# Performance work log

Measured on AMD Instinct MI355X. Metric: run time of the kernel, lower is better.

The kernel has to match this reference:

```python
import jax, jax.numpy as jnp
import numpy as np
from jax import lax

DIM = 192
HEADS = 8
HIDDEN = int(DIM * 2.66)  # 510
EPS_LN = 1e-5
EPS_NORM = 1e-12


def conv1x1(x, w):
    # x: (B,C,H,W), w: (O,I,1,1)
    return lax.conv_general_dilated(x, w, (1, 1), 'VALID',
                                    dimension_numbers=('NCHW', 'OIHW', 'NCHW'))


def dwconv3x3(x, w):
    # depthwise 3x3, padding=1; w: (C,1,3,3)
    c = x.shape[1]
    return lax.conv_general_dilated(x, w, (1, 1), 'SAME',
                                    dimension_numbers=('NCHW', 'OIHW', 'NCHW'),
                                    feature_group_count=c)


def layernorm_chan(x, weight, bias):
    # WithBias LayerNorm over channel dim of NCHW (matches to_3d -> LN(-1) -> to_4d)
    mu = jnp.mean(x, axis=1, keepdims=True)
    var = jnp.var(x, axis=1, keepdims=True)
    xn = (x - mu) * lax.rsqrt(var + EPS_LN)
    return xn * weight[None, :, None, None] + bias[None, :, None, None]


def l2norm(x):
    # F.normalize along last dim with eps=1e-12
    n = jnp.sqrt(jnp.sum(x * x, axis=-1, keepdims=True))
    return x / jnp.maximum(n, EPS_NORM)


def attention(x, temperature, w_qkv, w_qkv_dw, w_proj):
    b, c, h, w = x.shape
    hw = h * w
    head_dim = c // HEADS
    qkv = dwconv3x3(conv1x1(x, w_qkv), w_qkv_dw)  # (B, 3C, H, W)
    q, k, v = jnp.split(qkv, 3, axis=1)
    q = l2norm(q.reshape(b, HEADS, head_dim, hw))
    k = l2norm(k.reshape(b, HEADS, head_dim, hw))
    v = v.reshape(b, HEADS, head_dim, hw)
    # channel-wise attention: (B,H,d,d)
    attn = jnp.einsum('bhde,bhce->bhdc', q, k) * temperature[None]
    attn = jax.nn.softmax(attn, axis=-1)
    out = jnp.einsum('bhdc,bhce->bhde', attn, v).reshape(b, c, h, w)
    return conv1x1(out, w_proj)


def ffn(x, w_in, w_dw, w_out):
    x = conv1x1(x, w_in)                 # (B, 2*hidden, H, W)
    x = dwconv3x3(x, w_dw)
    x1, x2 = jnp.split(x, 2, axis=1)
    x = jax.nn.gelu(x1, approximate=False) * x2
    return conv1x1(x, w_out)


def setup_inputs() -> dict:
    key = jax.random.key(0)
    ks = jax.random.split(key, 8)
    b, c, h, w = 4, DIM, 128, 128
    s = 0.05
    return {
        'x': jax.random.normal(ks[0], (b, c, h, w), jnp.float32),
        'temperature': jnp.ones((HEADS, 1, 1), jnp.float32),
        'ln1_w': jnp.ones((c,), jnp.float32),
        'ln1_b': jnp.zeros((c,), jnp.float32),
        'ln2_w': jnp.ones((c,), jnp.float32),
        'ln2_b': jnp.zeros((c,), jnp.float32),
        'w_qkv': jax.random.normal(ks[1], (3 * c, c, 1, 1), jnp.float32) * s,
        'w_qkv_dw': jax.random.normal(ks[2], (3 * c, 1, 3, 3), jnp.float32) * s,
        'w_proj': jax.random.normal(ks[3], (c, c, 1, 1), jnp.float32) * s,
        'w_in': jax.random.normal(ks[4], (2 * HIDDEN, c, 1, 1), jnp.float32) * s,
        'w_dw': jax.random.normal(ks[5], (2 * HIDDEN, 1, 3, 3), jnp.float32) * s,
        'w_out_ffn': jax.random.normal(ks[6], (c, HIDDEN, 1, 1), jnp.float32) * s,
    }


def reference(x, temperature, ln1_w, ln1_b, ln2_w, ln2_b, w_qkv, w_qkv_dw,
              w_proj, w_in, w_dw, w_out_ffn):
    x = x + attention(layernorm_chan(x, ln1_w, ln1_b), temperature,
                      w_qkv, w_qkv_dw, w_proj)
    x = x + ffn(layernorm_chan(x, ln2_w, ln2_b), w_in, w_dw, w_out_ffn)
    return x
```

## Files before the change

kernel.cpp:

```cpp
#include <hip/hip_runtime.h>
#include <hip/hip_bf16.h>
#include <math.h>


#define HW_ 16384

typedef __attribute__((ext_vector_type(8))) short bf16x8;
typedef __attribute__((ext_vector_type(4))) float f32x4;
typedef __attribute__((ext_vector_type(16))) float f32x16;
typedef __attribute__((ext_vector_type(4))) int i32x4;

union Pack8 { __hip_bfloat16 h[8]; i32x4 v; };

__global__ __launch_bounds__(256) void convert_weights(
    const float* __restrict__ wqkv, const float* __restrict__ wproj,
    const float* __restrict__ win, const float* __restrict__ wout,
    __hip_bfloat16* __restrict__ oq, __hip_bfloat16* __restrict__ op,
    __hip_bfloat16* __restrict__ oi, __hip_bfloat16* __restrict__ oo) {
  const int i = blockIdx.x * 256 + threadIdx.x;
  if (i < 110592) oq[i] = __float2bfloat16(wqkv[i]);
  if (i < 36864)  op[i] = __float2bfloat16(wproj[i]);
  if (i < 196608) {
    int m = i / 192, k = i - m * 192;
    oi[i] = __float2bfloat16(m < 1020 ? win[m * 192 + k] : 0.f);
  }
  if (i < 98304) {
    int m = i >> 9, k = i & 511;
    oo[i] = __float2bfloat16(k < 510 ? wout[m * 510 + k] : 0.f);
  }
}

__global__ __launch_bounds__(256) void ln_t_kernel(
    const float* __restrict__ x, const float* __restrict__ w,
    const float* __restrict__ bi, __hip_bfloat16* __restrict__ yt) {
  const int b = blockIdx.y;
  x += (size_t)b * 192 * HW_;
  yt += (size_t)b * HW_ * 192;
  __shared__ float tile[192][68];
  __shared__ float psum[4][64], psq[4][64];
  __shared__ float mu_s[64], inv_s[64];
  const int tid = threadIdx.x;
  const int p0 = blockIdx.x * 64;
  for (int idx = tid; idx < 192 * 16; idx += 256) {
    int c = idx >> 4, p4 = idx & 15;
    f32x4 v = *(const f32x4*)(x + (size_t)c * HW_ + p0 + p4 * 4);
    *(f32x4*)&tile[c][p4 * 4] = v;
  }
  __syncthreads();
  const int tx = tid & 63, ty = tid >> 6;
  float s = 0.f, s2 = 0.f;
  for (int c = ty * 48; c < ty * 48 + 48; c++) {
    float v = tile[c][tx]; s += v; s2 += v * v;
  }
  psum[ty][tx] = s; psq[ty][tx] = s2;
  __syncthreads();
  if (ty == 0) {
    float ts = psum[0][tx] + psum[1][tx] + psum[2][tx] + psum[3][tx];
    float ts2 = psq[0][tx] + psq[1][tx] + psq[2][tx] + psq[3][tx];
    float mu = ts * (1.f / 192.f);
    float var = ts2 * (1.f / 192.f) - mu * mu;
    mu_s[tx] = mu; inv_s[tx] = rsqrtf(var + 1e-5f);
  }
  __syncthreads();
  for (int idx = tid; idx < 64 * 24; idx += 256) {
    int c8 = idx % 24, p = idx / 24;
    float mu = mu_s[p], inv = inv_s[p];
    Pack8 pk;
    #pragma unroll
    for (int u = 0; u < 8; u++) {
      int c = c8 * 8 + u;
      pk.h[u] = __float2bfloat16((tile[c][p] - mu) * inv * w[c] + bi[c]);
    }
    *(i32x4*)&yt[(size_t)(p0 + p) * 192 + c8 * 8] = pk.v;
  }
}

template <int EPI>
__global__ __launch_bounds__(256) void mfma_gemm(
    const __hip_bfloat16* __restrict__ A, const __hip_bfloat16* __restrict__ Bg,
    const float* __restrict__ Cres, void* __restrict__ Dout,
    int M, int N, int K, size_t Bstr, size_t Cstr, size_t Dstr) {
  const int z = blockIdx.z;
  const __hip_bfloat16* B = Bg + (size_t)z * Bstr;
  const float* C = Cres ? Cres + (size_t)z * Cstr : nullptr;
  __shared__ __align__(16) __hip_bfloat16 As[64][72];
  __shared__ __align__(16) __hip_bfloat16 Bs[128][72];
  const int tid = threadIdx.x;
  const int wave = tid >> 6, lane = tid & 63;
  const int quad = lane >> 4, lr = lane & 15;
  const int wm = (wave & 1) * 32, wn = (wave >> 1) * 64;
  const int row0 = blockIdx.x * 64, col0 = blockIdx.y * 128;

  f32x4 acc[2][4];
  #pragma unroll
  for (int i = 0; i < 2; i++)
    #pragma unroll
    for (int j = 0; j < 4; j++) acc[i][j] = (f32x4){0.f, 0.f, 0.f, 0.f};

  for (int k0 = 0; k0 < K; k0 += 64) {
    #pragma unroll
    for (int l = 0; l < 2; l++) {
      int t = tid + l * 256;
      int row = t >> 3, ch = t & 7;
      i32x4 v = *(const i32x4*)(A + (size_t)(row0 + row) * K + k0 + ch * 8);
      *(i32x4*)&As[row][ch * 8] = v;
    }
    #pragma unroll
    for (int l = 0; l < 4; l++) {
      int t = tid + l * 256;
      int row = t >> 3, ch = t & 7;
      i32x4 v = *(const i32x4*)(B + (size_t)(col0 + row) * K + k0 + ch * 8);
      *(i32x4*)&Bs[row][ch * 8] = v;
    }
    __syncthreads();
    #pragma unroll
    for (int ks = 0; ks < 2; ks++) {
      bf16x8 a0 = *(const bf16x8*)&As[wm + lr][ks * 32 + quad * 8];
      bf16x8 a1 = *(const bf16x8*)&As[wm + 16 + lr][ks * 32 + quad * 8];
      #pragma unroll
      for (int j = 0; j < 4; j++) {
        bf16x8 bb = *(const bf16x8*)&Bs[wn + j * 16 + lr][ks * 32 + quad * 8];
        acc[0][j] = __builtin_amdgcn_mfma_f32_16x16x32_bf16(a0, bb, acc[0][j], 0, 0, 0);
        acc[1][j] = __builtin_amdgcn_mfma_f32_16x16x32_bf16(a1, bb, acc[1][j], 0, 0, 0);
      }
    }
    __syncthreads();
  }

  #pragma unroll
  for (int i = 0; i < 2; i++) {
    #pragma unroll
    for (int r = 0; r < 4; r++) {
      int gm = row0 + wm + i * 16 + quad * 4 + r;
      if (gm >= M) continue;
      #pragma unroll
      for (int j = 0; j < 4; j++) {
        int gn = col0 + wn + j * 16 + lr;
        size_t idx = (size_t)gm * N + gn;
        if (EPI == 0) {
          (((__hip_bfloat16*)Dout) + (size_t)z * Dstr)[idx] = __float2bfloat16(acc[i][j][r]);
        } else {
          (((float*)Dout) + (size_t)z * Dstr)[idx] = acc[i][j][r] + C[idx];
        }
      }
    }
  }
}

__global__ __launch_bounds__(256) void dw_kernel(
    const __hip_bfloat16* __restrict__ in, const float* __restrict__ wdw,
    __hip_bfloat16* __restrict__ out, float* __restrict__ nrm2p) {
  const int b = blockIdx.z;
  in  += (size_t)b * 576 * HW_;
  out += (size_t)b * 576 * HW_;
  const int c = blockIdx.y;
  const int x8 = threadIdx.x & 15;
  const int y = blockIdx.x * 16 + (threadIdx.x >> 4);
  const __hip_bfloat16* ip = in + (size_t)c * HW_;
  const float* wp = wdw + c * 9;
  float wv[9];
  #pragma unroll
  for (int u = 0; u < 9; u++) wv[u] = wp[u];
  float acc[8];
  #pragma unroll
  for (int j = 0; j < 8; j++) acc[j] = 0.f;
  #pragma unroll
  for (int r = 0; r < 3; r++) {
    int yy = y + r - 1;
    if (yy < 0 || yy >= 128) continue;
    const __hip_bfloat16* rp = ip + yy * 128 + x8 * 8;
    Pack8 mid; mid.v = *(const i32x4*)rp;
    float row[10];
    row[0] = (x8 > 0) ? (float)rp[-1] : 0.f;
    #pragma unroll
    for (int u = 0; u < 8; u++) row[1 + u] = (float)mid.h[u];
    row[9] = (x8 < 15) ? (float)rp[8] : 0.f;
    const float wl = wv[r * 3], wc = wv[r * 3 + 1], wr = wv[r * 3 + 2];
    #pragma unroll
    for (int j = 0; j < 8; j++)
      acc[j] += wl * row[j] + wc * row[j + 1] + wr * row[j + 2];
  }
  Pack8 o;
  #pragma unroll
  for (int j = 0; j < 8; j++) o.h[j] = __float2bfloat16(acc[j]);
  *(i32x4*)(out + (size_t)c * HW_ + y * 128 + x8 * 8) = o.v;
  if (c < 384) {
    float s = 0.f;
    #pragma unroll
    for (int j = 0; j < 8; j++) s += acc[j] * acc[j];
    #pragma unroll
    for (int off = 32; off > 0; off >>= 1) s += __shfl_down(s, off, 64);
    __shared__ float wsum[4];
    const int lane = threadIdx.x & 63, wvi = threadIdx.x >> 6;
    if (lane == 0) wsum[wvi] = s;
    __syncthreads();
    if (threadIdx.x == 0)
      nrm2p[((size_t)b * 384 + c) * 8 + blockIdx.x] =
          wsum[0] + wsum[1] + wsum[2] + wsum[3];
  }
}

__global__ __launch_bounds__(256) void gram_kernel(
    const __hip_bfloat16* __restrict__ qkv, float* __restrict__ Gpart) {
  const int b = blockIdx.z;
  qkv   += (size_t)b * 576 * HW_;
  Gpart += (size_t)b * 32 * 8 * 576;
  const int h = blockIdx.x, chunk = blockIdx.y;
  const int tid = threadIdx.x;
  const int w = tid >> 6, lane = tid & 63;
  const int m = lane & 31;
  const int khalf = lane >> 5;
  const __hip_bfloat16* qb = qkv + (size_t)(h * 24) * HW_;
  const __hip_bfloat16* kb = qkv + (size_t)(192 + h * 24) * HW_;
  f32x16 acc;
  #pragma unroll
  for (int i = 0; i < 16; i++) acc[i] = 0.f;
  const int e0 = chunk * 512 + w * 128;
  #pragma unroll
  for (int j = 0; j < 8; j++) {
    const int k0 = e0 + j * 16 + khalf * 8;
    bf16x8 a = *(const bf16x8*)(qb + (size_t)m * HW_ + k0);
    bf16x8 bfr = *(const bf16x8*)(kb + (size_t)m * HW_ + k0);
    acc = __builtin_amdgcn_mfma_f32_32x32x16_bf16(a, bfr, acc, 0, 0, 0);
  }
  __shared__ float gs[4][576];
  #pragma unroll
  for (int r = 0; r < 16; r++) {
    int row = (r & 3) + 8 * (r >> 2) + 4 * khalf;
    if (row < 24 && m < 24) gs[w][row * 24 + m] = acc[r];
  }
  __syncthreads();
  float* gp = Gpart + (size_t)(chunk * 8 + h) * 576;
  for (int t = tid; t < 576; t += 256)
    gp[t] = gs[0][t] + gs[1][t] + gs[2][t] + gs[3][t];
}

__global__ __launch_bounds__(256) void softmax2_kernel(
    const float* __restrict__ Gpart, const float* __restrict__ nrm2p,
    const float* __restrict__ temp, float* __restrict__ P) {
  const int b = blockIdx.y;
  Gpart += (size_t)b * 32 * 8 * 576;
  nrm2p += (size_t)b * 384 * 8;
  P     += (size_t)b * 8 * 576;
  const int h = blockIdx.x;
  const int tid = threadIdx.x;
  __shared__ float Gs[576];
  __shared__ float nq[24], nk[24];
  for (int t = tid; t < 576; t += 256) {
    float s = 0.f;
    for (int ch = 0; ch < 32; ch++)
      s += Gpart[(size_t)(ch * 8 + h) * 576 + t];
    Gs[t] = s;
  }
  if (tid < 48) {
    const int r = (tid < 24) ? (h * 24 + tid) : (192 + h * 24 + tid - 24);
    float s = 0.f;
    #pragma unroll
    for (int j = 0; j < 8; j++) s += nrm2p[(size_t)r * 8 + j];
    float nv = fmaxf(sqrtf(s), 1e-12f);
    if (tid < 24) nq[tid] = nv; else nk[tid - 24] = nv;
  }
  __syncthreads();
  if (tid < 24) {
    const int d = tid;
    const float tp = temp[h];
    float row[24], mx = -1e30f;
    #pragma unroll
    for (int c = 0; c < 24; c++) {
      float v = Gs[d * 24 + c] * tp / (nq[d] * nk[c]);
      row[c] = v; mx = fmaxf(mx, v);
    }
    float s = 0.f;
    #pragma unroll
    for (int c = 0; c < 24; c++) { float e = expf(row[c] - mx); row[c] = e; s += e; }
    const float inv = 1.f / s;
    #pragma unroll
    for (int c = 0; c < 24; c++) P[h * 576 + d * 24 + c] = row[c] * inv;
  }
}

__global__ __launch_bounds__(256) void pv_kernel(
    const float* __restrict__ P, const __hip_bfloat16* __restrict__ qkv,
    __hip_bfloat16* __restrict__ yt) {
  const int b = blockIdx.z;
  P   += (size_t)b * 8 * 576;
  qkv += (size_t)b * 576 * HW_;
  yt  += (size_t)b * HW_ * 192;
  const int hh = blockIdx.x;
  const int e = blockIdx.y * 256 + threadIdx.x;
  __shared__ float Ps[576];
  for (int t = threadIdx.x; t < 576; t += 256) Ps[t] = P[hh * 576 + t];
  __syncthreads();
  const __hip_bfloat16* vb = qkv + (size_t)(384 + hh * 24) * HW_;
  float acc[24];
  #pragma unroll
  for (int d = 0; d < 24; d++) acc[d] = 0.f;
  for (int c = 0; c < 24; c++) {
    float v = (float)vb[(size_t)c * HW_ + e];
    #pragma unroll
    for (int d = 0; d < 24; d++) acc[d] += Ps[d * 24 + c] * v;
  }
  #pragma unroll
  for (int g = 0; g < 3; g++) {
    Pack8 pk;
    #pragma unroll
    for (int u = 0; u < 8; u++) pk.h[u] = __float2bfloat16(acc[g * 8 + u]);
    *(i32x4*)&yt[(size_t)e * 192 + hh * 24 + g * 8] = pk.v;
  }
}

__global__ __launch_bounds__(256) void dwg_t_kernel(
    const __hip_bfloat16* __restrict__ hsrc, const float* __restrict__ wdw,
    __hip_bfloat16* __restrict__ gt, int b0) {
  const int z = blockIdx.z;
  const int bb = b0 + z;
  const int yt = blockIdx.x >> 1, xh = blockIdx.x & 1;
  const int cz = blockIdx.y;
  const int tid = threadIdx.x;
  const int cl = tid >> 3, x8 = tid & 7;
  const int c = cz * 32 + cl;
  const int y0 = yt * 8;
  const int pxb = xh * 64 + x8 * 8;
  __shared__ __hip_bfloat16 sg[32][522];

  const bool active = (c < 510);
  const int ca = active ? c : 0;
  const __hip_bfloat16* ha = hsrc + ((size_t)bb * 1024 + ca) * HW_;
  const __hip_bfloat16* hb = hsrc + ((size_t)bb * 1024 + ca + 510) * HW_;
  float wva[9], wvb[9];
  #pragma unroll
  for (int u = 0; u < 9; u++) {
    wva[u] = active ? wdw[c * 9 + u] : 0.f;
    wvb[u] = active ? wdw[(c + 510) * 9 + u] : 0.f;
  }

  float aA[3][8], aB[3][8];
  #pragma unroll
  for (int s = 0; s < 3; s++)
    #pragma unroll
    for (int j = 0; j < 8; j++) { aA[s][j] = 0.f; aB[s][j] = 0.f; }

  #pragma unroll
  for (int i = 0; i < 10; i++) {
    const int ry = y0 - 1 + i;
    float ra[10], rb[10];
    if (ry >= 0 && ry < 128) {
      const int off = ry * 128 + pxb;
      Pack8 ma; ma.v = *(const i32x4*)(ha + off);
      Pack8 mb; mb.v = *(const i32x4*)(hb + off);
      ra[0] = (pxb > 0) ? (float)ha[off - 1] : 0.f;
      rb[0] = (pxb > 0) ? (float)hb[off - 1] : 0.f;
      #pragma unroll
      for (int u = 0; u < 8; u++) { ra[1 + u] = (float)ma.h[u]; rb[1 + u] = (float)mb.h[u]; }
      ra[9] = (pxb < 120) ? (float)ha[off + 8] : 0.f;
      rb[9] = (pxb < 120) ? (float)hb[off + 8] : 0.f;
    } else {
      #pragma unroll
      for (int u = 0; u < 10; u++) { ra[u] = 0.f; rb[u] = 0.f; }
    }
    #pragma unroll
    for (int r = 0; r < 3; r++) {
      const int lo = i - r;
      if (lo < 0 || lo >= 8) continue;
      const int s = lo % 3;
      const float a0 = wva[r * 3], a1 = wva[r * 3 + 1], a2 = wva[r * 3 + 2];
      const float b0w = wvb[r * 3], b1 = wvb[r * 3 + 1], b2 = wvb[r * 3 + 2];
      #pragma unroll
      for (int j = 0; j < 8; j++) {
        aA[s][j] += a0 * ra[j] + a1 * ra[j + 1] + a2 * ra[j + 2];
        aB[s][j] += b0w * rb[j] + b1 * rb[j + 1] + b2 * rb[j + 2];
      }
    }
    {
      const int lo = i - 2;
      if (lo >= 0 && lo < 8) {
        const int s = lo % 3;
        Pack8 o;
        #pragma unroll
        for (int j = 0; j < 8; j++) {
          float v = aA[s][j];
          float ge = 0.5f * v * (1.f + erff(v * 0.70710678118654752f));
          o.h[j] = __float2bfloat16(ge * aB[s][j]);
          aA[s][j] = 0.f; aB[s][j] = 0.f;
        }
        *(i32x4*)&sg[cl][lo * 64 + x8 * 8] = o.v;
      }
    }
  }
  __syncthreads();
  const int sp = tid >> 2, ch0 = (tid & 3) * 8;
  #pragma unroll
  for (int k = 0; k < 8; k++) {
    Pack8 o;
    #pragma unroll
    for (int u = 0; u < 8; u++) o.h[u] = sg[ch0 + u][k * 64 + sp];
    const int gp = (y0 + k) * 128 + xh * 64 + sp;
    *(i32x4*)&gt[((size_t)z * HW_ + gp) * 512 + cz * 32 + ch0] = o.v;
  }
}

extern "C" void kernel_launch(void* const* d_in, const int* in_sizes, int n_in,
                              void* d_out, int out_size, void* d_ws, size_t ws_size,
                              hipStream_t stream) {
  const float* x     = (const float*)d_in[0];
  const float* temp  = (const float*)d_in[1];
  const float* ln1w  = (const float*)d_in[2];
  const float* ln1b  = (const float*)d_in[3];
  const float* ln2w  = (const float*)d_in[4];
  const float* ln2b  = (const float*)d_in[5];
  const float* wqkv  = (const float*)d_in[6];
  const float* wqkvdw= (const float*)d_in[7];
  const float* wproj = (const float*)d_in[8];
  const float* win   = (const float*)d_in[9];
  const float* wdw   = (const float*)d_in[10];
  const float* wout  = (const float*)d_in[11];
  float* out = (float*)d_out;
  char* ws = (char*)d_ws;

  const int HW = 16384;
  const size_t HWC = (size_t)192 * HW;

  __hip_bfloat16* yt    = (__hip_bfloat16*)(ws + 0);
  __hip_bfloat16* qkva  = (__hip_bfloat16*)(ws + 25165824);
  __hip_bfloat16* qkvb  = (__hip_bfloat16*)(ws + 100663296);
  __hip_bfloat16* hbuf  = (__hip_bfloat16*)(ws + 25165824);
  float*          xa    = (float*)(ws + 176160768);
  __hip_bfloat16* gt    = (__hip_bfloat16*)(ws + 226492416);
  __hip_bfloat16* wqkvB = (__hip_bfloat16*)(ws + 260046848);
  __hip_bfloat16* wprojB= (__hip_bfloat16*)(ws + 260268032);
  __hip_bfloat16* winB  = (__hip_bfloat16*)(ws + 260341760);
  __hip_bfloat16* woutB = (__hip_bfloat16*)(ws + 260734976);
  float*          nrm2p = (float*)(ws + 260931584);
  float*          Gpart = (float*)(ws + 260980736);
  float*          P     = (float*)(ws + 263340032);

  convert_weights<<<768, 256, 0, stream>>>(wqkv, wproj, win, wout,
                                           wqkvB, wprojB, winB, woutB);

  ln_t_kernel<<<dim3(256, 4), 256, 0, stream>>>(x, ln1w, ln1b, yt);
  mfma_gemm<0><<<dim3(9, 128, 4), 256, 0, stream>>>(
      wqkvB, yt, nullptr, qkva, 576, HW, 192,
      (size_t)HW * 192, 0, (size_t)576 * HW);
  dw_kernel<<<dim3(8, 576, 4), 256, 0, stream>>>(qkva, wqkvdw, qkvb, nrm2p);
  gram_kernel<<<dim3(8, 32, 4), 256, 0, stream>>>(qkvb, Gpart);
  softmax2_kernel<<<dim3(8, 4), 256, 0, stream>>>(Gpart, nrm2p, temp, P);
  pv_kernel<<<dim3(8, 64, 4), 256, 0, stream>>>(P, qkvb, yt);
  mfma_gemm<1><<<dim3(3, 128, 4), 256, 0, stream>>>(
      wprojB, yt, x, xa, 192, HW, 192,
      (size_t)HW * 192, HWC, HWC);
  ln_t_kernel<<<dim3(256, 4), 256, 0, stream>>>(xa, ln2w, ln2b, yt);
  mfma_gemm<0><<<dim3(16, 128, 4), 256, 0, stream>>>(
      winB, yt, nullptr, hbuf, 1020, HW, 192,
      (size_t)HW * 192, 0, (size_t)1024 * HW);
  for (int half = 0; half < 2; half++) {
    const int b0 = half * 2;
    dwg_t_kernel<<<dim3(32, 16, 2), 256, 0, stream>>>(hbuf, wdw, gt, b0);
    mfma_gemm<1><<<dim3(3, 128, 2), 256, 0, stream>>>(
        woutB, gt, xa + (size_t)b0 * HWC, out + (size_t)b0 * HWC,
        192, HW, 512, (size_t)HW * 512, HWC, HWC);
  }
}
```

Baseline: 514.3 us.

## Keep activation tile resident in LDS and loop over weight tiles; swizzle LDS

Adds a GEMM kernel for K=192 that loads a 128-column activation tile into shared memory once and iterates over all weight row tiles. The next weight tile is prefetched into registers while the current one is computed. It replaces the qkv and FFN-in GEMMs with this kernel, so the activations are read from global memory once instead of once per M tile. Both GEMMs also switch from padded LDS rows to an XOR swizzle to avoid bank conflicts. The cost is a grid of only 512 blocks using about 72KB of LDS each, which lowers occupancy and parallelism.

```diff
diff --git a/kernel.cpp b/kernel.cpp
--- a/kernel.cpp
+++ b/kernel.cpp
@@ -75,6 +75,98 @@
   }
 }
 
+__global__ __launch_bounds__(256) void gemm_bstat(
+    const __hip_bfloat16* __restrict__ A, const __hip_bfloat16* __restrict__ Bg,
+    __hip_bfloat16* __restrict__ Dout, int Mtiles, size_t Bstr, size_t Dstr) {
+  const int z = blockIdx.y;
+  const __hip_bfloat16* B = Bg + (size_t)z * Bstr;
+  __hip_bfloat16* D = Dout + (size_t)z * Dstr;
+  const int col0 = blockIdx.x * 128;
+  __shared__ __align__(16) __hip_bfloat16 Bs[128][192];
+  __shared__ __align__(16) __hip_bfloat16 As[64][192];
+  const int tid = threadIdx.x;
+  const int wave = tid >> 6, lane = tid & 63;
+  const int quad = lane >> 4, lr = lane & 15;
+  const int wm = (wave & 1) * 32, wn = (wave >> 1) * 64;
+  const int lrx = lr & 7;
+
+  const int arow = tid >> 3, ach = tid & 7;
+  const int achs = ach ^ (arow & 7);
+
+  #pragma unroll
+  for (int l = 0; l < 4; l++) {
+    const int row = arow + 32 * l;
+    const __hip_bfloat16* bp = B + (size_t)(col0 + row) * 192;
+    #pragma unroll
+    for (int j = 0; j < 3; j++) {
+      i32x4 v = *(const i32x4*)(bp + (ach + 8 * j) * 8);
+      *(i32x4*)&Bs[row][(achs + 8 * j) * 8] = v;
+    }
+  }
+  i32x4 areg[6];
+  #pragma unroll
+  for (int l = 0; l < 2; l++)
+    #pragma unroll
+    for (int j = 0; j < 3; j++)
+      areg[l * 3 + j] = *(const i32x4*)(
+          A + (size_t)(arow + 32 * l) * 192 + (ach + 8 * j) * 8);
+  #pragma unroll
+  for (int l = 0; l < 2; l++)
+    #pragma unroll
+    for (int j = 0; j < 3; j++)
+      *(i32x4*)&As[arow + 32 * l][(achs + 8 * j) * 8] = areg[l * 3 + j];
+  __syncthreads();
+
+  for (int mt = 0; mt < Mtiles; mt++) {
+    const int row0 = mt * 64;
+    if (mt + 1 < Mtiles) {
+      const __hip_bfloat16* ap = A + (size_t)(mt + 1) * 64 * 192;
+      #pragma unroll
+      for (int l = 0; l < 2; l++)
+        #pragma unroll
+        for (int j = 0; j < 3; j++)
+          areg[l * 3 + j] = *(const i32x4*)(
+              ap + (size_t)(arow + 32 * l) * 192 + (ach + 8 * j) * 8);
+    }
+    f32x4 acc[2][4];
+    #pragma unroll
+    for (int i = 0; i < 2; i++)
+      #pragma unroll
+      for (int j = 0; j < 4; j++) acc[i][j] = (f32x4){0.f, 0.f, 0.f, 0.f};
+    #pragma unroll
+    for (int kc = 0; kc < 6; kc++) {
+      const int chq = ((kc * 4 + quad) ^ lrx) * 8;
+      bf16x8 a0 = *(const bf16x8*)&As[wm + lr][chq];
+      bf16x8 a1 = *(const bf16x8*)&As[wm + 16 + lr][chq];
+      #pragma unroll
+      for (int j = 0; j < 4; j++) {
+        bf16x8 bb = *(const bf16x8*)&Bs[wn + j * 16 + lr][chq];
+        acc[0][j] = __builtin_amdgcn_mfma_f32_16x16x32_bf16(a0, bb, acc[0][j], 0, 0, 0);
+        acc[1][j] = __builtin_amdgcn_mfma_f32_16x16x32_bf16(a1, bb, acc[1][j], 0, 0, 0);
+      }
+    }
+    #pragma unroll
+    for (int i = 0; i < 2; i++)
+      #pragma unroll
+      for (int r = 0; r < 4; r++) {
+        const int gm = row0 + wm + i * 16 + quad * 4 + r;
+        __hip_bfloat16* dp = D + (size_t)gm * HW_ + col0 + wn + lr;
+        #pragma unroll
+        for (int j = 0; j < 4; j++)
+          dp[j * 16] = __float2bfloat16(acc[i][j][r]);
+      }
+    __syncthreads();
+    if (mt + 1 < Mtiles) {
+      #pragma unroll
+      for (int l = 0; l < 2; l++)
+        #pragma unroll
+        for (int j = 0; j < 3; j++)
+          *(i32x4*)&As[arow + 32 * l][(achs + 8 * j) * 8] = areg[l * 3 + j];
+      __syncthreads();
+    }
+  }
+}
+
 template <int EPI>
 __global__ __launch_bounds__(256) void mfma_gemm(
     const __hip_bfloat16* __restrict__ A, const __hip_bfloat16* __restrict__ Bg,
@@ -83,11 +175,12 @@
   const int z = blockIdx.z;
   const __hip_bfloat16* B = Bg + (size_t)z * Bstr;
   const float* C = Cres ? Cres + (size_t)z * Cstr : nullptr;
-  __shared__ __align__(16) __hip_bfloat16 As[64][72];
-  __shared__ __align__(16) __hip_bfloat16 Bs[128][72];
+  __shared__ __align__(16) __hip_bfloat16 As[64][64];
+  __shared__ __align__(16) __hip_bfloat16 Bs[128][64];
   const int tid = threadIdx.x;
   const int wave = tid >> 6, lane = tid & 63;
   const int quad = lane >> 4, lr = lane & 15;
+  const int lrx = lr & 7;
   const int wm = (wave & 1) * 32, wn = (wave >> 1) * 64;
   const int row0 = blockIdx.x * 64, col0 = blockIdx.y * 128;
 
@@ -103,23 +196,24 @@
       int t = tid + l * 256;
       int row = t >> 3, ch = t & 7;
       i32x4 v = *(const i32x4*)(A + (size_t)(row0 + row) * K + k0 + ch * 8);
-      *(i32x4*)&As[row][ch * 8] = v;
+      *(i32x4*)&As[row][(ch ^ (row & 7)) * 8] = v;
     }
     #pragma unroll
     for (int l = 0; l < 4; l++) {
       int t = tid + l * 256;
       int row = t >> 3, ch = t & 7;
       i32x4 v = *(const i32x4*)(B + (size_t)(col0 + row) * K + k0 + ch * 8);
-      *(i32x4*)&Bs[row][ch * 8] = v;
+      *(i32x4*)&Bs[row][(ch ^ (row & 7)) * 8] = v;
     }
     __syncthreads();
     #pragma unroll
     for (int ks = 0; ks < 2; ks++) {
-      bf16x8 a0 = *(const bf16x8*)&As[wm + lr][ks * 32 + quad * 8];
-      bf16x8 a1 = *(const bf16x8*)&As[wm + 16 + lr][ks * 32 + quad * 8];
+      const int chq = ((ks * 4 + quad) ^ lrx) * 8;
+      bf16x8 a0 = *(const bf16x8*)&As[wm + lr][chq];
+      bf16x8 a1 = *(const bf16x8*)&As[wm + 16 + lr][chq];
       #pragma unroll
       for (int j = 0; j < 4; j++) {
-        bf16x8 bb = *(const bf16x8*)&Bs[wn + j * 16 + lr][ks * 32 + quad * 8];
+        bf16x8 bb = *(const bf16x8*)&Bs[wn + j * 16 + lr][chq];
         acc[0][j] = __builtin_amdgcn_mfma_f32_16x16x32_bf16(a0, bb, acc[0][j], 0, 0, 0);
         acc[1][j] = __builtin_amdgcn_mfma_f32_16x16x32_bf16(a1, bb, acc[1][j], 0, 0, 0);
       }
@@ -438,9 +532,8 @@
                                            wqkvB, wprojB, winB, woutB);
 
   ln_t_kernel<<<dim3(256, 4), 256, 0, stream>>>(x, ln1w, ln1b, yt);
-  mfma_gemm<0><<<dim3(9, 128, 4), 256, 0, stream>>>(
-      wqkvB, yt, nullptr, qkva, 576, HW, 192,
-      (size_t)HW * 192, 0, (size_t)576 * HW);
+  gemm_bstat<<<dim3(128, 4), 256, 0, stream>>>(
+      wqkvB, yt, qkva, 9, (size_t)HW * 192, (size_t)576 * HW);
   dw_kernel<<<dim3(8, 576, 4), 256, 0, stream>>>(qkva, wqkvdw, qkvb, nrm2p);
   gram_kernel<<<dim3(8, 32, 4), 256, 0, stream>>>(qkvb, Gpart);
   softmax2_kernel<<<dim3(8, 4), 256, 0, stream>>>(Gpart, nrm2p, temp, P);
@@ -449,9 +542,8 @@
       wprojB, yt, x, xa, 192, HW, 192,
       (size_t)HW * 192, HWC, HWC);
   ln_t_kernel<<<dim3(256, 4), 256, 0, stream>>>(xa, ln2w, ln2b, yt);
-  mfma_gemm<0><<<dim3(16, 128, 4), 256, 0, stream>>>(
-      winB, yt, nullptr, hbuf, 1020, HW, 192,
-      (size_t)HW * 192, 0, (size_t)1024 * HW);
+  gemm_bstat<<<dim3(128, 4), 256, 0, stream>>>(
+      winB, yt, hbuf, 16, (size_t)HW * 192, (size_t)1024 * HW);
   for (int half = 0; half < 2; half++) {
     const int b0 = half * 2;
     dwg_t_kernel<<<dim3(32, 16, 2), 256, 0, stream>>>(hbuf, wdw, gt, b0);
```

Result: faster. 486.6 us (-5.4%).
